# Performance work log

Measured on AMD Instinct MI355X. Metric: run time of the kernel, lower is better.

## Reference

```python
import jax, jax.numpy as jnp
import numpy as np

B = 8192          # batch
D = 256           # feature_dim
H = 64            # num attention heads
HD = D // H       # head_dim = 4
NC, NB, NF, NT = 2048, 2048, 512, 768
NCLS = 26
EPS = 1e-5


def _linear_params(k, out_d, in_d):
    s = 1.0 / np.sqrt(in_d)
    kw, kb = jax.random.split(k)
    W = jax.random.uniform(kw, (out_d, in_d), minval=-s, maxval=s, dtype=jnp.float32)
    b = jax.random.uniform(kb, (out_d,), minval=-s, maxval=s, dtype=jnp.float32)
    return W, b


def setup_inputs() -> dict:
    key = jax.random.key(0)
    ks = jax.random.split(key, 16)
    inp = {
        'x_context': jax.random.normal(ks[0], (B, NC), dtype=jnp.float32),
        'x_body':    jax.random.normal(ks[1], (B, NB), dtype=jnp.float32),
        'x_face':    jax.random.normal(ks[2], (B, NF), dtype=jnp.float32),
        'x_text':    jax.random.normal(ks[3], (B, NT), dtype=jnp.float32),
    }
    inp['Wc'], inp['bc'] = _linear_params(ks[4], D, NC)
    inp['Wb'], inp['bb'] = _linear_params(ks[5], D, NB)
    inp['Wf'], inp['bf'] = _linear_params(ks[6], D, NF)
    inp['Wt'], inp['bt'] = _linear_params(ks[7], D, NT)
    # MultiheadAttention packed in-proj (3D x D) and out-proj
    inp['in_w'], inp['in_b'] = _linear_params(ks[8], 3 * D, D)
    inp['out_w'], inp['out_b'] = _linear_params(ks[9], D, D)
    # gate MLP
    inp['Wg1'], inp['bg1'] = _linear_params(ks[10], D, D)
    inp['Wg2'], inp['bg2'] = _linear_params(ks[11], 1, D)
    # fusion head
    inp['W1'], inp['b1'] = _linear_params(ks[12], D, 4 * D)
    inp['gamma'] = jnp.ones((D,), dtype=jnp.float32)
    inp['beta'] = jnp.zeros((D,), dtype=jnp.float32)
    inp['W2'], inp['b2'] = _linear_params(ks[13], NCLS, D)
    return inp


def reference(x_context, x_body, x_face, x_text,
              Wc, bc, Wb, bb, Wf, bf, Wt, bt,
              in_w, in_b, out_w, out_b,
              Wg1, bg1, Wg2, bg2,
              W1, b1, gamma, beta, W2, b2):
    # per-modality projections -> [B, 4, D]
    f = jnp.stack([
        x_context @ Wc.T + bc,
        x_body    @ Wb.T + bb,
        x_face    @ Wf.T + bf,
        x_text    @ Wt.T + bt,
    ], axis=1)
    bsz = f.shape[0]

    # MultiheadAttention with seq_len=1 per token: softmax over a single key
    Wq, Wk, Wv = jnp.split(in_w, 3, axis=0)
    bq, bk, bv = jnp.split(in_b, 3)
    q = (f @ Wq.T + bq).reshape(bsz, 4, H, HD)
    k = (f @ Wk.T + bk).reshape(bsz, 4, H, HD)
    v = (f @ Wv.T + bv).reshape(bsz, 4, H, HD)
    scores = jnp.sum(q * k, axis=-1, keepdims=True) / np.sqrt(HD)  # [B,4,H,1]
    w = jax.nn.softmax(scores, axis=-1)                            # == 1 (single key)
    attn = (w * v).reshape(bsz, 4, D)
    self_out = attn @ out_w.T + out_b                              # [B,4,D]

    # cross attention: with seq_len=1 the output depends only on key/value,
    # so each (query i, key 3-j) call equals the self-style output of modality 3-j;
    # combining over the 4 key variants reduces to the mean over modalities.
    cross = jnp.mean(self_out, axis=1, keepdims=True)              # [B,1,D]

    gate = jax.nn.sigmoid(jax.nn.relu(self_out @ Wg1.T + bg1) @ Wg2.T + bg2)  # [B,4,1]
    combined = gate * self_out + (1.0 - gate) * cross              # [B,4,D]

    h = combined.reshape(bsz, 4 * D) @ W1.T + b1                   # [B,D]
    # BatchNorm1d (training-mode batch statistics, biased variance)
    mu = jnp.mean(h, axis=0)
    var = jnp.var(h, axis=0)
    h = (h - mu) / jnp.sqrt(var + EPS) * gamma + beta
    h = jax.nn.relu(h)                                             # dropout = identity (eval)
    return h @ W2.T + b2                                           # [B,26]
```

## Files before the change

kernel.cpp:

```cpp
#include <hip/hip_runtime.h>
#include <math.h>

typedef __attribute__((ext_vector_type(8))) short bf16x8;
typedef __attribute__((ext_vector_type(4))) short bf16x4;
typedef __attribute__((ext_vector_type(4))) float f32x4;
typedef unsigned short u16;
typedef unsigned int u32;

#define BSZ   8192
#define BN_EPS 1e-5f

__device__ inline u16 f2bf(float x) {
    u32 u = __float_as_uint(x);
    u32 r = (u + 0x7FFFu + ((u >> 16) & 1u)) >> 16;
    return (u16)r;
}
__device__ inline float bf2f_lo(u32 p) { return __uint_as_float(p << 16); }
__device__ inline float bf2f_hi(u32 p) { return __uint_as_float(p & 0xFFFF0000u); }

__device__ inline void async_g2l(const void* g, void* l) {
    __builtin_amdgcn_global_load_lds(
        (const __attribute__((address_space(1))) void*)g,
        (__attribute__((address_space(3))) void*)l, 16, 0, 0);
}

__global__ __launch_bounds__(256)
void wvo_kernel(const float* __restrict__ in_w, const float* __restrict__ in_b,
                const float* __restrict__ out_w, const float* __restrict__ out_b,
                float* __restrict__ wvo, float* __restrict__ bvo)
{
    const int i = blockIdx.x;
    const int j = threadIdx.x;
    const float* Wv = in_w + 512 * 256;
    float s = 0.f;
#pragma unroll 8
    for (int k = 0; k < 256; ++k)
        s = fmaf(out_w[i * 256 + k], Wv[k * 256 + j], s);
    wvo[i * 256 + j] = s;
    if (i == 0) {
        const float* bv = in_b + 512;
        float t = 0.f;
        for (int k = 0; k < 256; ++k)
            t = fmaf(out_w[j * 256 + k], bv[k], t);
        bvo[j] = t + out_b[j];
    }
}

__global__ __launch_bounds__(256)
void cvt_weights(const float* __restrict__ wvo, const float* __restrict__ Wc,
                 const float* __restrict__ Wb,  const float* __restrict__ Wf,
                 const float* __restrict__ Wt,  const float* __restrict__ Wg1,
                 const float* __restrict__ W1f, u16* __restrict__ dst)
{
    int gid = blockIdx.x * 256 + threadIdx.x;
    const float* src; u16* d; int loc;
    if      (gid <   8192) { src = wvo; d = dst + 0;       loc = gid; }
    else if (gid <  73728) { src = Wc;  d = dst + 65536;   loc = gid - 8192; }
    else if (gid < 139264) { src = Wb;  d = dst + 589824;  loc = gid - 73728; }
    else if (gid < 155648) { src = Wf;  d = dst + 1114112; loc = gid - 139264; }
    else if (gid < 180224) { src = Wt;  d = dst + 1245184; loc = gid - 155648; }
    else if (gid < 188416) { src = Wg1; d = dst + 1441792; loc = gid - 180224; }
    else                   { src = W1f; d = dst + 1507328; loc = gid - 188416; }
    const float4 v0 = *(const float4*)(src + (size_t)loc * 8);
    const float4 v1 = *(const float4*)(src + (size_t)loc * 8 + 4);
    uint4 o;
    o.x = (u32)f2bf(v0.x) | ((u32)f2bf(v0.y) << 16);
    o.y = (u32)f2bf(v0.z) | ((u32)f2bf(v0.w) << 16);
    o.z = (u32)f2bf(v1.x) | ((u32)f2bf(v1.y) << 16);
    o.w = (u32)f2bf(v1.z) | ((u32)f2bf(v1.w) << 16);
    *(uint4*)(d + (size_t)loc * 8) = o;
}

__global__ __launch_bounds__(256)
void gemm_proj(const float* __restrict__ A0, const float* __restrict__ A1,
               const float* __restrict__ A2, const float* __restrict__ A3,
               const u16* __restrict__ Wp0, const u16* __restrict__ Wp1,
               const u16* __restrict__ Wp2, const u16* __restrict__ Wp3,
               const float* __restrict__ b0, const float* __restrict__ b1,
               const float* __restrict__ b2, const float* __restrict__ b3,
               u16* __restrict__ fb)
{
    __shared__ u16 As[2][4096];
    __shared__ u16 Bs[2][16384];
    const int m = blockIdx.y;
    const float* A  = (m == 0) ? A0 : (m == 1) ? A1 : (m == 2) ? A2 : A3;
    const u16* Wp   = (m == 0) ? Wp0 : (m == 1) ? Wp1 : (m == 2) ? Wp2 : Wp3;
    const float* bi = (m == 0) ? b0 : (m == 1) ? b1 : (m == 2) ? b2 : b3;
    const int K     = (m == 0) ? 2048 : (m == 1) ? 2048 : (m == 2) ? 512 : 768;
    const int nt = K >> 6;

    const int t = threadIdx.x;
    const int w = t >> 6, l = t & 63;
    const int bm = blockIdx.x * 64;
    const int arow = t >> 2, akq = t & 3;

    float4 rA[4], rB[4];
    auto loadA = [&](int k0, float4* r) {
        const float* g = A + (size_t)(bm + arow) * K + k0 + akq * 16;
#pragma unroll
        for (int q = 0; q < 4; ++q) r[q] = *(const float4*)(g + q * 4);
    };
    auto writeA = [&](int buf, const float4* r) {
        bf16x8 p0, p1;
        p0[0] = (short)f2bf(r[0].x); p0[1] = (short)f2bf(r[0].y);
        p0[2] = (short)f2bf(r[0].z); p0[3] = (short)f2bf(r[0].w);
        p0[4] = (short)f2bf(r[1].x); p0[5] = (short)f2bf(r[1].y);
        p0[6] = (short)f2bf(r[1].z); p0[7] = (short)f2bf(r[1].w);
        p1[0] = (short)f2bf(r[2].x); p1[1] = (short)f2bf(r[2].y);
        p1[2] = (short)f2bf(r[2].z); p1[3] = (short)f2bf(r[2].w);
        p1[4] = (short)f2bf(r[3].x); p1[5] = (short)f2bf(r[3].y);
        p1[6] = (short)f2bf(r[3].z); p1[7] = (short)f2bf(r[3].w);
        char* abw = (char*)As[buf];
        *(bf16x8*)(abw + arow * 128 + (((akq * 2 + 0) ^ (arow & 7)) << 4)) = p0;
        *(bf16x8*)(abw + arow * 128 + (((akq * 2 + 1) ^ (arow & 7)) << 4)) = p1;
    };
    auto issueB = [&](int k0, int buf) {
#pragma unroll
        for (int it = 0; it < 8; ++it) {
            const int n  = it * 32 + w * 8 + (l >> 3);
            const int ch = (l & 7) ^ (n & 7);
            async_g2l(Wp + (size_t)n * K + k0 + ch * 8, Bs[buf] + it * 2048 + w * 512);
        }
    };

    f32x4 acc[4][4];
    const f32x4 z = {0.f, 0.f, 0.f, 0.f};
#pragma unroll
    for (int i = 0; i < 4; ++i)
#pragma unroll
        for (int j = 0; j < 4; ++j) acc[i][j] = z;

    auto compute = [&](const char* abr, const char* bbr) {
#pragma unroll
        for (int kk = 0; kk < 2; ++kk) {
            bf16x8 af[4], bq[4];
            const int ch = kk * 4 + (l >> 4);
#pragma unroll
            for (int i = 0; i < 4; ++i) {
                const int fr = i * 16 + (l & 15);
                af[i] = *(const bf16x8*)(abr + fr * 128 + ((ch ^ (fr & 7)) << 4));
            }
#pragma unroll
            for (int j = 0; j < 4; ++j) {
                const int n = w * 64 + j * 16 + (l & 15);
                bq[j] = *(const bf16x8*)(bbr + n * 128 + ((ch ^ (n & 7)) << 4));
            }
#pragma unroll
            for (int i = 0; i < 4; ++i)
#pragma unroll
                for (int j = 0; j < 4; ++j)
                    acc[i][j] = __builtin_amdgcn_mfma_f32_16x16x32_bf16(
                        af[i], bq[j], acc[i][j], 0, 0, 0);
        }
    };

    loadA(0, rA);
    writeA(0, rA);
    issueB(0, 0);
    loadA(64, rB);
    issueB(64, 1);
    loadA(128, rA);
    asm volatile("s_waitcnt vmcnt(16) lgkmcnt(0)" ::: "memory");
    __builtin_amdgcn_sched_barrier(0);
    __builtin_amdgcn_s_barrier();

    for (int t0 = 0; t0 < nt; t0 += 2) {
        compute((const char*)As[0], (const char*)Bs[0]);
        writeA(1, rB);
        __builtin_amdgcn_s_barrier();
        if (t0 + 3 < nt) {
            loadA((t0 + 3) * 64, rB);
            issueB((t0 + 2) * 64, 0);
            asm volatile("s_waitcnt vmcnt(12) lgkmcnt(0)" ::: "memory");
        } else if (t0 + 2 < nt) {
            issueB((t0 + 2) * 64, 0);
            asm volatile("s_waitcnt vmcnt(8) lgkmcnt(0)" ::: "memory");
        } else {
            asm volatile("s_waitcnt vmcnt(0) lgkmcnt(0)" ::: "memory");
        }
        __builtin_amdgcn_sched_barrier(0);
        __builtin_amdgcn_s_barrier();

        compute((const char*)As[1], (const char*)Bs[1]);
        if (t0 + 2 < nt) writeA(0, rA);
        __builtin_amdgcn_s_barrier();
        if (t0 + 4 < nt) {
            loadA((t0 + 4) * 64, rA);
            issueB((t0 + 3) * 64, 1);
            asm volatile("s_waitcnt vmcnt(12) lgkmcnt(0)" ::: "memory");
        } else if (t0 + 3 < nt) {
            issueB((t0 + 3) * 64, 1);
            asm volatile("s_waitcnt vmcnt(8) lgkmcnt(0)" ::: "memory");
        } else {
            asm volatile("s_waitcnt vmcnt(0) lgkmcnt(0)" ::: "memory");
        }
        __builtin_amdgcn_sched_barrier(0);
        __builtin_amdgcn_s_barrier();
    }

#pragma unroll
    for (int j = 0; j < 4; ++j) {
        const int col = w * 64 + j * 16 + (l & 15);
        const float bv = bi[col];
#pragma unroll
        for (int i = 0; i < 4; ++i)
#pragma unroll
            for (int r = 0; r < 4; ++r) {
                const int rt = i * 16 + ((l >> 4) << 2) + r;
                fb[((size_t)(bm + rt) * 4 + m) * 256 + col] = f2bf(acc[i][j][r] + bv);
            }
    }
}

__global__ __launch_bounds__(256)
void fused_sgc(const u16* __restrict__ fb, const u16* __restrict__ wvo_bf,
               const float* __restrict__ bvo,
               const u16* __restrict__ wg1_bf, const float* __restrict__ bg1,
               const float* __restrict__ wg2, const float* __restrict__ bg2,
               u16* __restrict__ comb)
{
    __shared__ u16 FS[8192];
    __shared__ u16 Bs[2][8192];
    __shared__ float gp[4][32];
    __shared__ float gate_s[32];
    const int t = threadIdx.x, w = t >> 6, l = t & 63;
    const int bm = blockIdx.x * 32;
    char* const fs = (char*)FS;

#pragma unroll
    for (int it = 0; it < 4; ++it) {
        const int r0 = (w * 4 + it) * 2;
        const int row = r0 + (l >> 5);
        const int ch = (l & 31) ^ (row & 7);
        async_g2l(fb + (size_t)(bm + row) * 256 + ch * 8, FS + r0 * 256);
    }
    auto issueB = [&](const u16* Wp, int k0, int buf) {
#pragma unroll
        for (int it = 0; it < 4; ++it) {
            const int n0 = (w * 4 + it) * 16;
            async_g2l(Wp + (size_t)(n0 + (l >> 2)) * 256 + k0 + (l & 3) * 8,
                      Bs[buf] + n0 * 32);
        }
    };
    issueB(wvo_bf, 0, 0);
    __syncthreads();

    const f32x4 z = {0.f, 0.f, 0.f, 0.f};

    f32x4 acc[2][4];
#pragma unroll
    for (int i = 0; i < 2; ++i)
#pragma unroll
        for (int j = 0; j < 4; ++j) acc[i][j] = z;

    for (int ks = 0; ks < 8; ++ks) {
        const int cur = ks & 1;
        if (ks < 7) issueB(wvo_bf, (ks + 1) * 32, cur ^ 1);
        else        issueB(wg1_bf, 0, 0);
        bf16x8 af[2], bq[4];
#pragma unroll
        for (int i = 0; i < 2; ++i) {
            const int row = i * 16 + (l & 15);
            af[i] = *(const bf16x8*)(fs + row * 512 +
                      (((ks * 4 + (l >> 4)) ^ (row & 7)) << 4));
        }
#pragma unroll
        for (int j = 0; j < 4; ++j)
            bq[j] = *(const bf16x8*)((char*)Bs[cur] +
                      (w * 64 + j * 16 + (l & 15)) * 64 + (l >> 4) * 16);
#pragma unroll
        for (int i = 0; i < 2; ++i)
#pragma unroll
            for (int j = 0; j < 4; ++j)
                acc[i][j] = __builtin_amdgcn_mfma_f32_16x16x32_bf16(
                    af[i], bq[j], acc[i][j], 0, 0, 0);
        __syncthreads();
    }

#pragma unroll
    for (int j = 0; j < 4; ++j) {
        const int col = w * 64 + j * 16 + (l & 15);
        const float bv = bvo[col];
#pragma unroll
        for (int i = 0; i < 2; ++i)
#pragma unroll
            for (int r = 0; r < 4; ++r) {
                const int rt = i * 16 + ((l >> 4) << 2) + r;
                *(u16*)(fs + rt * 512 + (((col >> 3) ^ (rt & 7)) << 4) + (col & 7) * 2)
                    = f2bf(acc[i][j][r] + bv);
            }
    }
    __syncthreads();

    f32x4 g2[2][4];
#pragma unroll
    for (int i = 0; i < 2; ++i)
#pragma unroll
        for (int j = 0; j < 4; ++j) g2[i][j] = z;

    for (int ks = 0; ks < 8; ++ks) {
        const int cur = ks & 1;
        if (ks < 7) issueB(wg1_bf, (ks + 1) * 32, cur ^ 1);
        bf16x8 af[2], bq[4];
#pragma unroll
        for (int i = 0; i < 2; ++i) {
            const int row = i * 16 + (l & 15);
            af[i] = *(const bf16x8*)(fs + row * 512 +
                      (((ks * 4 + (l >> 4)) ^ (row & 7)) << 4));
        }
#pragma unroll
        for (int j = 0; j < 4; ++j)
            bq[j] = *(const bf16x8*)((char*)Bs[cur] +
                      (w * 64 + j * 16 + (l & 15)) * 64 + (l >> 4) * 16);
#pragma unroll
        for (int i = 0; i < 2; ++i)
#pragma unroll
            for (int j = 0; j < 4; ++j)
                g2[i][j] = __builtin_amdgcn_mfma_f32_16x16x32_bf16(
                    af[i], bq[j], g2[i][j], 0, 0, 0);
        __syncthreads();
    }

    {
        float s[2][4];
#pragma unroll
        for (int i = 0; i < 2; ++i)
#pragma unroll
            for (int r = 0; r < 4; ++r) s[i][r] = 0.f;
#pragma unroll
        for (int j = 0; j < 4; ++j) {
            const int col = w * 64 + j * 16 + (l & 15);
            const float bv = bg1[col], wv = wg2[col];
#pragma unroll
            for (int i = 0; i < 2; ++i)
#pragma unroll
                for (int r = 0; r < 4; ++r)
                    s[i][r] += fmaxf(g2[i][j][r] + bv, 0.f) * wv;
        }
#pragma unroll
        for (int off = 1; off < 16; off <<= 1)
#pragma unroll
            for (int i = 0; i < 2; ++i)
#pragma unroll
                for (int r = 0; r < 4; ++r)
                    s[i][r] += __shfl_xor(s[i][r], off);
        if ((l & 15) == 0) {
#pragma unroll
            for (int i = 0; i < 2; ++i)
#pragma unroll
                for (int r = 0; r < 4; ++r)
                    gp[w][i * 16 + ((l >> 4) << 2) + r] = s[i][r];
        }
    }
    __syncthreads();
    if (t < 32) {
        const float g = gp[0][t] + gp[1][t] + gp[2][t] + gp[3][t] + bg2[0];
        gate_s[t] = 1.f / (1.f + expf(-g));
    }
    __syncthreads();

    u32* const comb32 = (u32*)comb;
    const int p2 = t & 127;
    const int gh = t >> 7;
#pragma unroll
    for (int gg = 0; gg < 4; ++gg) {
        const int g = gh * 4 + gg;
        const int d0 = p2 * 2;
        float lo4[4], hi4[4], gv[4];
#pragma unroll
        for (int mm = 0; mm < 4; ++mm) {
            const int row = g * 4 + mm;
            const u32 v = *(const u32*)(fs + row * 512 +
                            (((d0 >> 3) ^ (row & 7)) << 4) + (d0 & 7) * 2);
            lo4[mm] = bf2f_lo(v); hi4[mm] = bf2f_hi(v);
            gv[mm] = gate_s[g * 4 + mm];
        }
        const float cl = 0.25f * (lo4[0] + lo4[1] + lo4[2] + lo4[3]);
        const float ch = 0.25f * (hi4[0] + hi4[1] + hi4[2] + hi4[3]);
#pragma unroll
        for (int mm = 0; mm < 4; ++mm) {
            const float ol = gv[mm] * lo4[mm] + (1.f - gv[mm]) * cl;
            const float oh = gv[mm] * hi4[mm] + (1.f - gv[mm]) * ch;
            comb32[(size_t)(bm + g * 4 + mm) * 128 + p2] =
                (u32)f2bf(ol) | ((u32)f2bf(oh) << 16);
        }
    }
}

__global__ __launch_bounds__(256)
void gemm_w1(const u16* __restrict__ combp, const u16* __restrict__ w1p,
             const float* __restrict__ b1p, float* __restrict__ h)
{
    __shared__ u16 As[2][1024];
    __shared__ u16 Bs[2][8192];
    const int t = threadIdx.x, w = t >> 6, l = t & 63;
    const int bm = blockIdx.x * 32;
    const int nt = 32;

    auto issueA = [&](int k0, int buf) {
        if (w < 2) {
            const int r0 = w * 16;
            async_g2l(combp + (size_t)(bm + r0 + (l >> 2)) * 1024 + k0 + (l & 3) * 8,
                      As[buf] + r0 * 32);
        }
    };
    auto issueB = [&](int k0, int buf) {
#pragma unroll
        for (int it = 0; it < 4; ++it) {
            const int n0 = (w * 4 + it) * 16;
            async_g2l(w1p + (size_t)(n0 + (l >> 2)) * 1024 + k0 + (l & 3) * 8,
                      Bs[buf] + n0 * 32);
        }
    };

    f32x4 acc[2][4];
    const f32x4 z = {0.f, 0.f, 0.f, 0.f};
#pragma unroll
    for (int i = 0; i < 2; ++i)
#pragma unroll
        for (int j = 0; j < 4; ++j) acc[i][j] = z;

    issueA(0, 0);
    issueB(0, 0);
    __syncthreads();

    for (int t0 = 0; t0 < nt; ++t0) {
        const int cur = t0 & 1;
        if (t0 + 1 < nt) { issueA((t0 + 1) * 32, cur ^ 1); issueB((t0 + 1) * 32, cur ^ 1); }
        const char* ab = (const char*)As[cur];
        const char* bb = (const char*)Bs[cur];
        bf16x8 af[2], bq[4];
#pragma unroll
        for (int i = 0; i < 2; ++i)
            af[i] = *(const bf16x8*)(ab + (i * 16 + (l & 15)) * 64 + (l >> 4) * 16);
#pragma unroll
        for (int j = 0; j < 4; ++j)
            bq[j] = *(const bf16x8*)(bb + (w * 64 + j * 16 + (l & 15)) * 64 + (l >> 4) * 16);
#pragma unroll
        for (int i = 0; i < 2; ++i)
#pragma unroll
            for (int j = 0; j < 4; ++j)
                acc[i][j] = __builtin_amdgcn_mfma_f32_16x16x32_bf16(
                    af[i], bq[j], acc[i][j], 0, 0, 0);
        __syncthreads();
    }

#pragma unroll
    for (int j = 0; j < 4; ++j) {
        const int col = w * 64 + j * 16 + (l & 15);
        const float bv = b1p[col];
#pragma unroll
        for (int i = 0; i < 2; ++i)
#pragma unroll
            for (int r = 0; r < 4; ++r) {
                const int rt = i * 16 + ((l >> 4) << 2) + r;
                h[(size_t)(bm + rt) * 256 + col] = acc[i][j][r] + bv;
            }
    }
}

__global__ __launch_bounds__(256)
void bn_part(const float* __restrict__ h, float* __restrict__ psum,
             float* __restrict__ psq)
{
    const int p = blockIdx.x;
    const int d = threadIdx.x;
    float s = 0.f, q = 0.f;
#pragma unroll 8
    for (int r = 0; r < 32; ++r) {
        const float v = h[((size_t)p * 32 + r) * 256 + d];
        s += v;
        q = fmaf(v, v, q);
    }
    psum[p * 256 + d] = s;
    psq[p * 256 + d]  = q;
}

__global__ __launch_bounds__(256)
void bn_fin(const float* __restrict__ psum, const float* __restrict__ psq,
            const float* __restrict__ gamma, const float* __restrict__ beta,
            float* __restrict__ scale, float* __restrict__ shift)
{
    const int d = threadIdx.x;
    float s = 0.f, q = 0.f;
#pragma unroll 8
    for (int p = 0; p < 256; ++p) { s += psum[p * 256 + d]; q += psq[p * 256 + d]; }
    const float mu  = s * (1.f / BSZ);
    const float var = q * (1.f / BSZ) - mu * mu;
    const float inv = rsqrtf(var + BN_EPS);
    const float sc  = gamma[d] * inv;
    scale[d] = sc;
    shift[d] = beta[d] - mu * sc;
}

__global__ __launch_bounds__(256)
void final_kernel(const float* __restrict__ h, const float* __restrict__ scale,
                  const float* __restrict__ shift, const float* __restrict__ W2,
                  const float* __restrict__ b2, float* __restrict__ out)
{
    __shared__ float W2s[26][260];
    __shared__ float scs[256], shs[256];
    const int t = threadIdx.x;
    for (int u = t; u < 26 * 256; u += 256) {
        const int c = u >> 8, n = u & 255;
        W2s[c][(n >> 6) * 65 + (n & 63)] = W2[u];
    }
    scs[t] = scale[t];
    shs[t] = shift[t];
    __syncthreads();

    const int r = blockIdx.x * 64 + (t >> 2);
    const int p = t & 3;
    float acc[26];
#pragma unroll
    for (int c = 0; c < 26; ++c) acc[c] = 0.f;
    const float* hr = h + (size_t)r * 256 + p * 64;
#pragma unroll
    for (int i4 = 0; i4 < 16; ++i4) {
        const float4 v4 = *(const float4*)(hr + i4 * 4);
#pragma unroll
        for (int q = 0; q < 4; ++q) {
            const int i = i4 * 4 + q;
            const int n = p * 64 + i;
            const float vv = (q == 0) ? v4.x : (q == 1) ? v4.y : (q == 2) ? v4.z : v4.w;
            const float v = fmaxf(fmaf(vv, scs[n], shs[n]), 0.f);
            const int sw = p * 65 + i;
#pragma unroll
            for (int c = 0; c < 26; ++c)
                acc[c] = fmaf(v, W2s[c][sw], acc[c]);
        }
    }
#pragma unroll
    for (int off = 1; off < 4; off <<= 1)
#pragma unroll
        for (int c = 0; c < 26; ++c)
            acc[c] += __shfl_xor(acc[c], off);
    if (p == 0) {
#pragma unroll
        for (int c = 0; c < 26; ++c)
            out[(size_t)r * 26 + c] = acc[c] + b2[c];
    }
}

extern "C" void kernel_launch(void* const* d_in, const int* in_sizes, int n_in,
                              void* d_out, int out_size, void* d_ws, size_t ws_size,
                              hipStream_t stream)
{
    const float* x_ctx  = (const float*)d_in[0];
    const float* x_body = (const float*)d_in[1];
    const float* x_face = (const float*)d_in[2];
    const float* x_text = (const float*)d_in[3];
    const float* Wc = (const float*)d_in[4];  const float* bc = (const float*)d_in[5];
    const float* Wb = (const float*)d_in[6];  const float* bb = (const float*)d_in[7];
    const float* Wf = (const float*)d_in[8];  const float* bf = (const float*)d_in[9];
    const float* Wt = (const float*)d_in[10]; const float* bt = (const float*)d_in[11];
    const float* in_w  = (const float*)d_in[12]; const float* in_b  = (const float*)d_in[13];
    const float* out_w = (const float*)d_in[14]; const float* out_b = (const float*)d_in[15];
    const float* Wg1 = (const float*)d_in[16]; const float* bg1 = (const float*)d_in[17];
    const float* Wg2 = (const float*)d_in[18]; const float* bg2 = (const float*)d_in[19];
    const float* W1  = (const float*)d_in[20]; const float* b1  = (const float*)d_in[21];
    const float* gamma = (const float*)d_in[22]; const float* beta = (const float*)d_in[23];
    const float* W2  = (const float*)d_in[24]; const float* b2  = (const float*)d_in[25];

    char* wsb = (char*)d_ws;
    u16*   f_bf  = (u16*)(wsb + 0);
    u16*   comb  = f_bf;
    float* h     = (float*)(wsb + (16u << 20));
    u16*   wpb   = (u16*)(wsb + (32u << 20));
    float* wvo   = (float*)(wsb + (36u << 20));
    float* bvo   = (float*)(wsb + (36u << 20) + 262144);
    float* psum  = (float*)(wsb + (37u << 20));
    float* psq   = (float*)(wsb + (37u << 20) + 262144);
    float* scale = (float*)(wsb + (37u << 20) + 524288);
    float* shift = (float*)(wsb + (37u << 20) + 528384);

    u16* wvo_bf = wpb + 0;
    u16* wc_bf  = wpb + 65536;
    u16* wb_bf  = wpb + 589824;
    u16* wf_bf  = wpb + 1114112;
    u16* wt_bf  = wpb + 1245184;
    u16* wg1_bf = wpb + 1441792;
    u16* w1_bf  = wpb + 1507328;

    wvo_kernel<<<256, 256, 0, stream>>>(in_w, in_b, out_w, out_b, wvo, bvo);
    cvt_weights<<<864, 256, 0, stream>>>(wvo, Wc, Wb, Wf, Wt, Wg1, W1, wpb);

    gemm_proj<<<dim3(128, 4), 256, 0, stream>>>(x_ctx, x_body, x_face, x_text,
                                                wc_bf, wb_bf, wf_bf, wt_bf,
                                                bc, bb, bf, bt, f_bf);

    fused_sgc<<<1024, 256, 0, stream>>>(f_bf, wvo_bf, bvo, wg1_bf, bg1,
                                        Wg2, bg2, comb);

    gemm_w1<<<256, 256, 0, stream>>>(comb, w1_bf, b1, h);

    bn_part<<<256, 256, 0, stream>>>(h, psum, psq);
    bn_fin<<<1, 256, 0, stream>>>(psum, psq, gamma, beta, scale, shift);
    final_kernel<<<128, 256, 0, stream>>>(h, scale, shift, W2, b2, (float*)d_out);
}
```

Measured before the change: 153.9 us.

## Pre-convert activations to bf16 and use async-LDS GEMM for projections

Adds a separate pass that converts the four fp32 input matrices to bf16 in workspace, then runs a projection GEMM that loads both A and B tiles directly into LDS with global_load_lds instead of converting A in registers. It is meant to simplify the GEMM's A-load path and let both operands use async copies. In exchange it adds a full extra read of about 168MB fp32 and a write of 84MB bf16, plus a reread in the GEMM, and it only runs when the workspace is at least 140MB.

```diff
diff --git a/kernel.cpp b/kernel.cpp
--- a/kernel.cpp
+++ b/kernel.cpp
@@ -72,6 +72,120 @@
 }
 
 __global__ __launch_bounds__(256)
+void cvt_x(const float* __restrict__ x0, const float* __restrict__ x1,
+           const float* __restrict__ x2, const float* __restrict__ x3,
+           u16* __restrict__ xbf)
+{
+    const long long NU0 = 4194304;
+    const long long NU1 = NU0 + 4194304;
+    const long long NU2 = NU1 + 1048576;
+    const long long NUT = NU2 + 1572864;
+    const long long stride = (long long)gridDim.x * 256;
+    for (long long u = (long long)blockIdx.x * 256 + threadIdx.x; u < NUT; u += stride) {
+        const float* src; u16* dst; long long lu;
+        if      (u < NU0) { src = x0; dst = xbf;            lu = u; }
+        else if (u < NU1) { src = x1; dst = xbf + 16777216; lu = u - NU0; }
+        else if (u < NU2) { src = x2; dst = xbf + 33554432; lu = u - NU1; }
+        else              { src = x3; dst = xbf + 37748736; lu = u - NU2; }
+        const float4 v = *(const float4*)(src + lu * 4);
+        uint2 o;
+        o.x = (u32)f2bf(v.x) | ((u32)f2bf(v.y) << 16);
+        o.y = (u32)f2bf(v.z) | ((u32)f2bf(v.w) << 16);
+        *(uint2*)(dst + lu * 4) = o;
+    }
+}
+
+__global__ __launch_bounds__(256)
+void gemm_projb(const u16* __restrict__ xbf, const u16* __restrict__ wpb,
+                const float* __restrict__ b0, const float* __restrict__ b1,
+                const float* __restrict__ b2, const float* __restrict__ b3,
+                u16* __restrict__ fb)
+{
+    __shared__ u16 As[2][4096];
+    __shared__ u16 Bs[2][16384];
+    const int m = blockIdx.y;
+    const u16* A  = xbf + ((m == 0) ? 0 : (m == 1) ? 16777216 :
+                           (m == 2) ? 33554432 : 37748736);
+    const u16* Wp = wpb + ((m == 0) ? 65536 : (m == 1) ? 589824 :
+                           (m == 2) ? 1114112 : 1245184);
+    const float* bi = (m == 0) ? b0 : (m == 1) ? b1 : (m == 2) ? b2 : b3;
+    const int K     = (m == 0) ? 2048 : (m == 1) ? 2048 : (m == 2) ? 512 : 768;
+    const int nt = K >> 6;
+
+    const int t = threadIdx.x;
+    const int w = t >> 6, l = t & 63;
+    const int bm = blockIdx.x * 64;
+
+    auto issueAB = [&](int k0, int buf) {
+#pragma unroll
+        for (int it = 0; it < 8; ++it) {
+            const int n  = it * 32 + w * 8 + (l >> 3);
+            const int ch = (l & 7) ^ (n & 7);
+            async_g2l(Wp + (size_t)n * K + k0 + ch * 8, Bs[buf] + it * 2048 + w * 512);
+        }
+#pragma unroll
+        for (int it = 0; it < 2; ++it) {
+            const int row = it * 32 + w * 8 + (l >> 3);
+            const int ch  = (l & 7) ^ (row & 7);
+            async_g2l(A + (size_t)(bm + row) * K + k0 + ch * 8,
+                      As[buf] + it * 2048 + w * 512);
+        }
+    };
+
+    f32x4 acc[4][4];
+    const f32x4 z = {0.f, 0.f, 0.f, 0.f};
+#pragma unroll
+    for (int i = 0; i < 4; ++i)
+#pragma unroll
+        for (int j = 0; j < 4; ++j) acc[i][j] = z;
+
+    issueAB(0, 0);
+    __syncthreads();
+
+    for (int t0 = 0; t0 < nt; ++t0) {
+        const int cur = t0 & 1;
+        if (t0 + 1 < nt) issueAB((t0 + 1) * 64, cur ^ 1);
+        const char* abr = (const char*)As[cur];
+        const char* bbr = (const char*)Bs[cur];
+#pragma unroll
+        for (int kk = 0; kk < 2; ++kk) {
+            bf16x8 af[4], bq[4];
+            const int ch = kk * 4 + (l >> 4);
+#pragma unroll
+            for (int i = 0; i < 4; ++i) {
+                const int fr = i * 16 + (l & 15);
+                af[i] = *(const bf16x8*)(abr + fr * 128 + ((ch ^ (fr & 7)) << 4));
+            }
+#pragma unroll
+            for (int j = 0; j < 4; ++j) {
+                const int n = w * 64 + j * 16 + (l & 15);
+                bq[j] = *(const bf16x8*)(bbr + n * 128 + ((ch ^ (n & 7)) << 4));
+            }
+#pragma unroll
+            for (int i = 0; i < 4; ++i)
+#pragma unroll
+                for (int j = 0; j < 4; ++j)
+                    acc[i][j] = __builtin_amdgcn_mfma_f32_16x16x32_bf16(
+                        af[i], bq[j], acc[i][j], 0, 0, 0);
+        }
+        __syncthreads();
+    }
+
+#pragma unroll
+    for (int j = 0; j < 4; ++j) {
+        const int col = w * 64 + j * 16 + (l & 15);
+        const float bv = bi[col];
+#pragma unroll
+        for (int i = 0; i < 4; ++i)
+#pragma unroll
+            for (int r = 0; r < 4; ++r) {
+                const int rt = i * 16 + ((l >> 4) << 2) + r;
+                fb[((size_t)(bm + rt) * 4 + m) * 256 + col] = f2bf(acc[i][j][r] + bv);
+            }
+    }
+}
+
+__global__ __launch_bounds__(256)
 void gemm_proj(const float* __restrict__ A0, const float* __restrict__ A1,
                const float* __restrict__ A2, const float* __restrict__ A3,
                const u16* __restrict__ Wp0, const u16* __restrict__ Wp1,
@@ -563,16 +677,20 @@
     const float* W2  = (const float*)d_in[24]; const float* b2  = (const float*)d_in[25];
 
     char* wsb = (char*)d_ws;
-    u16*   f_bf  = (u16*)(wsb + 0);
+    const bool big = ws_size >= (140ull << 20);
+    char* base = wsb + (big ? (96ull << 20) : 0);
+
+    u16*   xbf   = (u16*)wsb;
+    u16*   f_bf  = (u16*)(base + 0);
     u16*   comb  = f_bf;
-    float* h     = (float*)(wsb + (16u << 20));
-    u16*   wpb   = (u16*)(wsb + (32u << 20));
-    float* wvo   = (float*)(wsb + (36u << 20));
-    float* bvo   = (float*)(wsb + (36u << 20) + 262144);
-    float* psum  = (float*)(wsb + (37u << 20));
-    float* psq   = (float*)(wsb + (37u << 20) + 262144);
-    float* scale = (float*)(wsb + (37u << 20) + 524288);
-    float* shift = (float*)(wsb + (37u << 20) + 528384);
+    float* h     = (float*)(base + (16u << 20));
+    u16*   wpb   = (u16*)(base + (32u << 20));
+    float* wvo   = (float*)(base + (36u << 20));
+    float* bvo   = (float*)(base + (36u << 20) + 262144);
+    float* psum  = (float*)(base + (37u << 20));
+    float* psq   = (float*)(base + (37u << 20) + 262144);
+    float* scale = (float*)(base + (37u << 20) + 524288);
+    float* shift = (float*)(base + (37u << 20) + 528384);
 
     u16* wvo_bf = wpb + 0;
     u16* wc_bf  = wpb + 65536;
@@ -585,9 +703,14 @@
     wvo_kernel<<<256, 256, 0, stream>>>(in_w, in_b, out_w, out_b, wvo, bvo);
     cvt_weights<<<864, 256, 0, stream>>>(wvo, Wc, Wb, Wf, Wt, Wg1, W1, wpb);
 
-    gemm_proj<<<dim3(128, 4), 256, 0, stream>>>(x_ctx, x_body, x_face, x_text,
-                                                wc_bf, wb_bf, wf_bf, wt_bf,
-                                                bc, bb, bf, bt, f_bf);
+    if (big) {
+        cvt_x<<<2048, 256, 0, stream>>>(x_ctx, x_body, x_face, x_text, xbf);
+        gemm_projb<<<dim3(128, 4), 256, 0, stream>>>(xbf, wpb, bc, bb, bf, bt, f_bf);
+    } else {
+        gemm_proj<<<dim3(128, 4), 256, 0, stream>>>(x_ctx, x_body, x_face, x_text,
+                                                    wc_bf, wb_bf, wf_bf, wt_bf,
+                                                    bc, bb, bf, bt, f_bf);
+    }
 
     fused_sgc<<<1024, 256, 0, stream>>>(f_bf, wvo_bf, bvo, wg1_bf, bg1,
                                         Wg2, bg2, comb);
```

After: 191.4 us. 1.24x slower.
